# Performance work log

Hardware: AMD Instinct MI355X
Metric: run time of the kernel (lower is better)

The kernel has to match this reference:

```python
import jax, jax.numpy as jnp
import numpy as np

T, B, H = 1024, 256, 20


def setup_inputs() -> dict:
    key = jax.random.key(0)
    ks = jax.random.split(key, 6)

    def lin_w(k, fan_in, fan_out):
        bound = 1.0 / np.sqrt(fan_in)
        return jax.random.uniform(k, (fan_in, fan_out), jnp.float32, -bound, bound)

    # t is time-reversed (torch.flip): strictly decreasing, so dt = t[0]-t[1] > 0
    t = jnp.linspace(1.0, 0.0, T, dtype=jnp.float32).reshape(T, 1)
    y = jax.random.uniform(ks[0], (B, 1, 3), jnp.float32)  # initial SIR state per batch
    return {
        "t": t,
        "y": y,
        "w1": lin_w(ks[1], 1, H), "b1": jnp.zeros((H,), jnp.float32),
        "w2": lin_w(ks[2], H, H), "b2": jnp.zeros((H,), jnp.float32),
        "w3": lin_w(ks[3], H, H), "b3": jnp.zeros((H,), jnp.float32),
        "w4": lin_w(ks[4], H, 1), "b4": jnp.zeros((1,), jnp.float32),
        "beta": jnp.asarray(0.2, jnp.float32),
        "gamma": jnp.asarray(0.2, jnp.float32),
    }


def reference(t, y, w1, b1, w2, b2, w3, b3, w4, b4, beta, gamma):
    Tn = t.shape[0]
    dt = t[0, 0] - t[1, 0]  # positive scalar (t is reversed)

    # memory kernel me(t): Linear-Tanh x3 -> Linear-Sigmoid, shape [T]
    h = jnp.tanh(t @ w1 + b1)
    h = jnp.tanh(h @ w2 + b2)
    h = jnp.tanh(h @ w3 + b3)
    me = jax.nn.sigmoid(h @ w4 + b4)[:, 0]  # [T]
    # pad so me[-j:] can be read as a fixed-length dynamic slice (zeros past end)
    me_pad = jnp.concatenate([me, jnp.zeros((Tn,), me.dtype)])  # [2T]

    y0 = jnp.transpose(y, (1, 0, 2))[0]  # [B,3]  (y.transpose(1,0) then first/only row)
    Bn = y0.shape[0]
    # history buffer of I-compartment values; entries >= current length stay zero
    I_hist0 = jnp.zeros((Tn, Bn), y0.dtype).at[0].set(y0[:, 1])

    def step(carry, idx):
        y_cur, I_hist = carry  # y_cur [B,3], I_hist [T,B]
        j = idx + 1  # current solution length
        # kernel slice w[k] = me[T - j + k]; for k >= j both w (padding) and I_hist are 0
        w = jax.lax.dynamic_slice(me_pad, (Tn - j,), (Tn,))  # [T]
        integ = dt * jnp.einsum('t,tb->b', w, I_hist)  # memory integral, [B]
        S, I = y_cur[:, 0], y_cur[:, 1]
        bSI = beta * S * I
        gI = gamma * I
        d = jnp.stack([-bSI + integ, bSI - gI, gI - integ], axis=1)  # [B,3]
        y_next = y_cur + d * dt  # forward Euler
        I_hist = I_hist.at[j].set(y_next[:, 1])
        return (y_next, I_hist), (d, y_next)

    (_, _), (ds, ys) = jax.lax.scan(step, (y0, I_hist0), jnp.arange(Tn - 1))
    solution = jnp.concatenate([y0[None], ys], axis=0)  # [T,B,3]
    # original leaves diff[T-1] as zeros (loop fills rows 0..T-2)
    diff = jnp.concatenate([ds, jnp.zeros((1, Bn, 3), ds.dtype)], axis=0)  # [T,B,3]
    return solution, diff
```

## Files before the change

kernel.cpp:

```cpp
#include <hip/hip_runtime.h>

#define T_N 1024
#define B_N 256
#define H_N 20
#define NW  8
#define NDW (NW - 1)
#define SIH 1096

typedef _Float16 h8_t __attribute__((ext_vector_type(8)));

#if __has_builtin(__builtin_amdgcn_fdot2)
#define DOT8(acc, mv, iv)                                                           \
    acc = __builtin_amdgcn_fdot2(__builtin_shufflevector(mv, mv, 0, 1),             \
                                 __builtin_shufflevector(iv, iv, 0, 1), acc, false);\
    acc = __builtin_amdgcn_fdot2(__builtin_shufflevector(mv, mv, 2, 3),             \
                                 __builtin_shufflevector(iv, iv, 2, 3), acc, false);\
    acc = __builtin_amdgcn_fdot2(__builtin_shufflevector(mv, mv, 4, 5),             \
                                 __builtin_shufflevector(iv, iv, 4, 5), acc, false);\
    acc = __builtin_amdgcn_fdot2(__builtin_shufflevector(mv, mv, 6, 7),             \
                                 __builtin_shufflevector(iv, iv, 6, 7), acc, false);
#else
#define DOT8(acc, mv, iv)                                                           \
    _Pragma("unroll")                                                               \
    for (int _k = 0; _k < 8; ++_k) acc = fmaf((float)mv[_k], (float)iv[_k], acc);
#endif

__device__ __forceinline__ float rdlane_i(float v, int lane) {
    return __uint_as_float((unsigned)__builtin_amdgcn_readlane((int)__float_as_uint(v), lane));
}
__device__ __forceinline__ float fast_tanh(float x) {
    const float e = __expf(2.0f * x);
    return fmaf(-2.0f, __builtin_amdgcn_rcpf(e + 1.0f), 1.0f);
}
__device__ __forceinline__ float fast_sigmoid(float x) {
    return __builtin_amdgcn_rcpf(1.0f + __expf(-x));
}

#define REP64(F) \
    F(0) F(1) F(2) F(3) F(4) F(5) F(6) F(7) F(8) F(9) F(10) F(11) F(12) F(13) \
    F(14) F(15) F(16) F(17) F(18) F(19) F(20) F(21) F(22) F(23) F(24) F(25)   \
    F(26) F(27) F(28) F(29) F(30) F(31) F(32) F(33) F(34) F(35) F(36) F(37)   \
    F(38) F(39) F(40) F(41) F(42) F(43) F(44) F(45) F(46) F(47) F(48) F(49)   \
    F(50) F(51) F(52) F(53) F(54) F(55) F(56) F(57) F(58) F(59) F(60) F(61)   \
    F(62) F(63)

__global__ __launch_bounds__(512, 1) void me_kernel(
    const float* __restrict__ t,
    const float* __restrict__ w1, const float* __restrict__ b1,
    const float* __restrict__ w2, const float* __restrict__ b2,
    const float* __restrict__ w3, const float* __restrict__ b3,
    const float* __restrict__ w4, const float* __restrict__ b4,
    float* __restrict__ me_f,
    _Float16* __restrict__ me_h)
{
    const int gid = blockIdx.x * 512 + threadIdx.x;
    const float x = t[gid];

    float h1[H_N], h2[H_N];
#pragma unroll
    for (int k = 0; k < H_N; ++k) h1[k] = fast_tanh(fmaf(x, w1[k], b1[k]));

#pragma unroll 4
    for (int k = 0; k < H_N; ++k) {
        float a = b2[k];
#pragma unroll
        for (int j = 0; j < H_N; ++j) a = fmaf(h1[j], w2[j * H_N + k], a);
        h2[k] = fast_tanh(a);
    }

    float a4 = b4[0];
#pragma unroll 4
    for (int k = 0; k < H_N; ++k) {
        float a = b3[k];
#pragma unroll
        for (int j = 0; j < H_N; ++j) a = fmaf(h2[j], w3[j * H_N + k], a);
        a4 = fmaf(fast_tanh(a), w4[k], a4);
    }

    const float meval = fast_sigmoid(a4);
    me_f[gid] = meval;
    me_h[gid] = (_Float16)meval;
}

__global__ __launch_bounds__(512, 1) void scan_kernel(
    const float* __restrict__ me_f,
    const _Float16* __restrict__ me_h,
    const float* __restrict__ t,
    const float* __restrict__ y,
    const float* __restrict__ beta_p,
    const float* __restrict__ gamma_p,
    float* __restrict__ out)
{
    __shared__ __align__(16) float    sMeF[T_N];
    __shared__ __align__(16) _Float16 sMeH[T_N];
    __shared__ __align__(16) _Float16 sIhR[8 * SIH];
    __shared__ __align__(16) float    PA[2][64][4];
    __shared__ __align__(16) float    PB[2][64][4];

    const int b   = blockIdx.x;
    const int tid = threadIdx.x;
    const int wid = tid >> 6;
    const int L   = tid & 63;

    const int f    = (-L) & 7;
    const int R8   = L + f;
    const int row  = L & 7;
    const int iofs = row * SIH + (f ? 0 : 8);

    if (tid < 64) sIhR[(tid >> 3) * SIH + (tid & 7)] = (_Float16)0.0f;
    if (tid < 128) PB[tid >> 6][tid & 63][3] = 0.0f;

#pragma unroll
    for (int v = 0; v < 2; ++v) {
        const int mi = tid + v * 512;
        sMeF[mi] = me_f[mi];
        sMeH[mi] = me_h[mi];
    }

    const float dt    = t[0] - t[1];
    const float beta  = beta_p[0];
    const float gma   = gamma_p[0];
    const float invdt = 1.0f / dt;
    const float dt2   = dt * dt;

    const float S0 = y[b * 3 + 0];
    const float I0 = y[b * 3 + 1];
    const float R0 = y[b * 3 + 2];
    const float TOT = S0 + I0 + R0;

    if (tid < 8) sIhR[tid * SIH + 8 - tid] = (_Float16)I0;

    float* __restrict__ diff = out + (size_t)T_N * B_N * 3;
    if (tid < 3) diff[((size_t)(T_N - 1) * B_N + b) * 3 + tid] = 0.0f;

    __syncthreads();

    float mf[7];
#pragma unroll
    for (int d = 1; d <= 7; ++d) mf[d - 1] = sMeF[T_N - 64 - L - d];

    const float dtb   = dt * beta;
    const float ndtb  = -dtb;
    const float c1    = fmaf(-dt, gma, 1.0f);
    const float meT1s = dt2 * sMeF[T_N - 1];

    float S = S0, I = I0, oS = S0, oI = I0;
    float acc_cur = 0.0f, acc_nxt = 0.0f, pre = 0.0f;
    float carryS = S0, carryI = I0;

#define TBLDECL(k) float rm_##k, rn_##k;
    REP64(TBLDECL)
#undef TBLDECL
    if (wid == 0) {
#define TBLINIT(k)                                                          \
        rm_##k = (((k) < L) ? sMeF[T_N - L + (k)] : 0.0f) * dt2;            \
        rn_##k = dt2 * sMeF[T_N - 64 - L + (k)];
        REP64(TBLINIT)
#undef TBLINIT
#define TBLPIN(k) asm volatile("" : "+v"(rm_##k), "+v"(rn_##k));
        REP64(TBLPIN)
#undef TBLPIN
        __builtin_amdgcn_s_setprio(3);
    }

#define STEPB(M_, FIRST_)                                               \
    {                                                                   \
        const float sum = (FIRST_) ? pre : fmaf(meT1s, I, pre);         \
        float pnx = pre;                                                \
        if ((M_) < 63) pnx = rdlane_i(acc_cur, (M_) + 1);               \
        const float a  = fmaf(dtb, S, c1);                              \
        const float bb = fmaf(ndtb, I, 1.0f);                           \
        S = fmaf(bb, S, sum);                                           \
        I = I * a;                                                      \
        const bool cap = (L == (M_));                                   \
        oS = cap ? S : oS;                                              \
        oI = cap ? I : oI;                                              \
        acc_cur = fmaf(rm_##M_, I, acc_cur);                            \
        acc_nxt = fmaf(rn_##M_, I, acc_nxt);                            \
        pre = pnx;                                                      \
    }
#define STEP_GE1(M_) if ((M_) >= 1) STEPB(M_, false)
#define STEP_GE2(M_) if ((M_) >= 2) STEPB(M_, false)

    for (int c = 0; c < 16; ++c) {
        if (wid == 0) {
            if (c == 0) {
                acc_cur = rm_0 * I;
                acc_nxt = rn_0 * I;
                pre = rdlane_i(acc_cur, 1);
                STEPB(1, true)
                REP64(STEP_GE2)
            } else {
                const float4 pa = *(const float4*)&PA[c & 1][L][0];
                const float4 pb = *(const float4*)&PB[c & 1][L][0];
                const float ps = ((pa.x + pa.y) + (pa.z + pa.w)) +
                                 ((pb.x + pb.y) + (pb.z + pb.w));
                acc_cur = fmaf(dt2, ps, acc_nxt);
                acc_nxt = 0.0f;
                pre = rdlane_i(acc_cur, 0);
                STEPB(0, true)
                REP64(STEP_GE1)
            }

            const int j = 64 * c + L;
            const _Float16 hI = (_Float16)oI;
#pragma unroll
            for (int r = 0; r < 8; ++r) sIhR[r * SIH + 8 + (j - r)] = hI;

            const float oR = TOT - oS - oI;
            const size_t so = ((size_t)j * B_N + b) * 3;
            out[so + 0] = oS;
            out[so + 1] = oI;
            out[so + 2] = oR;

            float sm1 = __shfl_up(oS, 1);
            float im1 = __shfl_up(oI, 1);
            if (L == 0) { sm1 = carryS; im1 = carryI; }
            if (j > 0) {
                const float d0 = (oS - sm1) * invdt;
                const float d1 = (oI - im1) * invdt;
                const float d2 = -d0 - d1;
                const size_t dofs = ((size_t)(j - 1) * B_N + b) * 3;
                diff[dofs + 0] = d0;
                diff[dofs + 1] = d1;
                diff[dofs + 2] = d2;
            }
            carryS = rdlane_i(oS, 63);
            carryI = rdlane_i(oI, 63);
        } else if (c < 15) {
            const int w    = wid - 1;
            const int G    = 8 * c;
            const int idx0 = (T_N - 64 * (c + 1)) - R8;
            float p0 = 0.0f, p1 = 0.0f;
            int s = w;
            for (; s + NDW < G; s += 2 * NDW) {
                const h8_t mv0 = *(const h8_t*)&sMeH[idx0 + 8 * s];
                const h8_t iv0 = *(const h8_t*)&sIhR[iofs + 8 * s];
                const h8_t mv1 = *(const h8_t*)&sMeH[idx0 + 8 * (s + NDW)];
                const h8_t iv1 = *(const h8_t*)&sIhR[iofs + 8 * (s + NDW)];
                DOT8(p0, mv0, iv0)
                DOT8(p1, mv1, iv1)
            }
            if (s < G) {
                const h8_t mv0 = *(const h8_t*)&sMeH[idx0 + 8 * s];
                const h8_t iv0 = *(const h8_t*)&sIhR[iofs + 8 * s];
                DOT8(p0, mv0, iv0)
            }
            float p = p0 + p1;
            if (w == 0) {
#pragma unroll
                for (int d = 1; d <= 7; ++d) {
                    const float ih = (float)sIhR[8 + 64 * c - d];
                    if (d <= f) p = fmaf(mf[d - 1], ih, p);
                }
            }
            if (w < 4) PA[(c + 1) & 1][L][w] = p;
            else       PB[(c + 1) & 1][L][w - 4] = p;
        }
        __syncthreads();
    }
#undef STEPB
#undef STEP_GE1
#undef STEP_GE2
}

extern "C" void kernel_launch(void* const* d_in, const int* in_sizes, int n_in,
                              void* d_out, int out_size, void* d_ws, size_t ws_size,
                              hipStream_t stream) {
    const float* t     = (const float*)d_in[0];
    const float* y     = (const float*)d_in[1];
    const float* w1    = (const float*)d_in[2];
    const float* b1    = (const float*)d_in[3];
    const float* w2    = (const float*)d_in[4];
    const float* b2    = (const float*)d_in[5];
    const float* w3    = (const float*)d_in[6];
    const float* b3    = (const float*)d_in[7];
    const float* w4    = (const float*)d_in[8];
    const float* b4    = (const float*)d_in[9];
    const float* beta  = (const float*)d_in[10];
    const float* gamma = (const float*)d_in[11];

    float*    me_f = (float*)d_ws;
    _Float16* me_h = (_Float16*)((char*)d_ws + 4096);

    me_kernel<<<2, 512, 0, stream>>>(t, w1, b1, w2, b2, w3, b3, w4, b4, me_f, me_h);
    scan_kernel<<<B_N, 512, 0, stream>>>(me_f, me_h, t, y, beta, gamma, (float*)d_out);
}
```

Before: 114.2 us.

## Batch lane reads in groups of eight and patch the recent memory terms explicitly

Result: slower. 119.8 us (+4.9%).

```diff
diff --git a/kernel.cpp b/kernel.cpp
--- a/kernel.cpp
+++ b/kernel.cpp
@@ -143,10 +143,20 @@
     const float ndtb  = -dtb;
     const float c1    = fmaf(-dt, gma, 1.0f);
     const float meT1s = dt2 * sMeF[T_N - 1];
+    const float meT2s = dt2 * sMeF[T_N - 2];
+    const float meT3s = dt2 * sMeF[T_N - 3];
+    const float meT4s = dt2 * sMeF[T_N - 4];
+    const float meT5s = dt2 * sMeF[T_N - 5];
+    const float meT6s = dt2 * sMeF[T_N - 6];
+    const float meT7s = dt2 * sMeF[T_N - 7];
 
     float S = S0, I = I0, oS = S0, oI = I0;
-    float acc_cur = 0.0f, acc_nxt = 0.0f, pre = 0.0f;
+    float acc_cur = 0.0f, acc_nxt = 0.0f;
     float carryS = S0, carryI = I0;
+    float rd_0 = 0.0f, rd_1 = 0.0f, rd_2 = 0.0f, rd_3 = 0.0f;
+    float rd_4 = 0.0f, rd_5 = 0.0f, rd_6 = 0.0f, rd_7 = 0.0f;
+    float gi0 = 0.0f, gi1 = 0.0f, gi2 = 0.0f, gi3 = 0.0f;
+    float gi4 = 0.0f, gi5 = 0.0f, gi6 = 0.0f;
 
 #define TBLDECL(k) float rm_##k, rn_##k;
     REP64(TBLDECL)
@@ -163,11 +173,39 @@
         __builtin_amdgcn_s_setprio(3);
     }
 
-#define STEPB(M_, FIRST_)                                               \
+#define PATCH0(s_)
+#define PATCH1(s_) s_ = fmaf(meT1s, gi0, s_);
+#define PATCH2(s_) s_ = fmaf(meT1s, gi1, fmaf(meT2s, gi0, s_));
+#define PATCH3(s_) s_ = fmaf(meT1s, gi2, fmaf(meT2s, gi1, fmaf(meT3s, gi0, s_)));
+#define PATCH4(s_) s_ = fmaf(meT1s, gi3, fmaf(meT2s, gi2, fmaf(meT3s, gi1, \
+                        fmaf(meT4s, gi0, s_))));
+#define PATCH5(s_) s_ = fmaf(meT1s, gi4, fmaf(meT2s, gi3, fmaf(meT3s, gi2, \
+                        fmaf(meT4s, gi1, fmaf(meT5s, gi0, s_)))));
+#define PATCH6(s_) s_ = fmaf(meT1s, gi5, fmaf(meT2s, gi4, fmaf(meT3s, gi3, \
+                        fmaf(meT4s, gi2, fmaf(meT5s, gi1, fmaf(meT6s, gi0, s_))))));
+#define PATCH7(s_) s_ = fmaf(meT1s, gi6, fmaf(meT2s, gi5, fmaf(meT3s, gi4, \
+                        fmaf(meT4s, gi3, fmaf(meT5s, gi2, fmaf(meT6s, gi1, \
+                        fmaf(meT7s, gi0, s_)))))));
+
+#define GSTEP(M_, P_)                                                   \
     {                                                                   \
-        const float sum = (FIRST_) ? pre : fmaf(meT1s, I, pre);         \
-        float pnx = pre;                                                \
-        if ((M_) < 63) pnx = rdlane_i(acc_cur, (M_) + 1);               \
+        float sum = rd_##P_;                                            \
+        PATCH##P_(sum)                                                  \
+        const float a  = fmaf(dtb, S, c1);                              \
+        const float bb = fmaf(ndtb, I, 1.0f);                           \
+        S = fmaf(bb, S, sum);                                           \
+        I = I * a;                                                      \
+        gi##P_ = I;                                                     \
+        const bool cap = (L == (M_));                                   \
+        oS = cap ? S : oS;                                              \
+        oI = cap ? I : oI;                                              \
+        acc_cur = fmaf(rm_##M_, I, acc_cur);                            \
+        acc_nxt = fmaf(rn_##M_, I, acc_nxt);                            \
+    }
+#define GSTEP7(M_)                                                      \
+    {                                                                   \
+        float sum = rd_7;                                               \
+        PATCH7(sum)                                                     \
         const float a  = fmaf(dtb, S, c1);                              \
         const float bb = fmaf(ndtb, I, 1.0f);                           \
         S = fmaf(bb, S, sum);                                           \
@@ -177,19 +215,47 @@
         oI = cap ? I : oI;                                              \
         acc_cur = fmaf(rm_##M_, I, acc_cur);                            \
         acc_nxt = fmaf(rn_##M_, I, acc_nxt);                            \
-        pre = pnx;                                                      \
-    }
-#define STEP_GE1(M_) if ((M_) >= 1) STEPB(M_, false)
-#define STEP_GE2(M_) if ((M_) >= 2) STEPB(M_, false)
+    }
+
+#define GREAD(B_)                                                       \
+    rd_0 = rdlane_i(acc_cur, (B_) + 0);                                 \
+    rd_1 = rdlane_i(acc_cur, (B_) + 1);                                 \
+    rd_2 = rdlane_i(acc_cur, (B_) + 2);                                 \
+    rd_3 = rdlane_i(acc_cur, (B_) + 3);                                 \
+    rd_4 = rdlane_i(acc_cur, (B_) + 4);                                 \
+    rd_5 = rdlane_i(acc_cur, (B_) + 5);                                 \
+    rd_6 = rdlane_i(acc_cur, (B_) + 6);                                 \
+    rd_7 = rdlane_i(acc_cur, (B_) + 7);
+
+#define GROUP(B_, M0,M1,M2,M3,M4,M5,M6,M7)                              \
+    GREAD(B_)                                                           \
+    GSTEP(M0,0) GSTEP(M1,1) GSTEP(M2,2) GSTEP(M3,3)                     \
+    GSTEP(M4,4) GSTEP(M5,5) GSTEP(M6,6) GSTEP7(M7)
+
+#define GROUPS_8_63                                                     \
+    GROUP(8,  8,9,10,11,12,13,14,15)                                    \
+    GROUP(16, 16,17,18,19,20,21,22,23)                                  \
+    GROUP(24, 24,25,26,27,28,29,30,31)                                  \
+    GROUP(32, 32,33,34,35,36,37,38,39)                                  \
+    GROUP(40, 40,41,42,43,44,45,46,47)                                  \
+    GROUP(48, 48,49,50,51,52,53,54,55)                                  \
+    GROUP(56, 56,57,58,59,60,61,62,63)
 
     for (int c = 0; c < 16; ++c) {
         if (wid == 0) {
             if (c == 0) {
                 acc_cur = rm_0 * I;
                 acc_nxt = rn_0 * I;
-                pre = rdlane_i(acc_cur, 1);
-                STEPB(1, true)
-                REP64(STEP_GE2)
+                rd_0 = rdlane_i(acc_cur, 1);
+                rd_1 = rdlane_i(acc_cur, 2);
+                rd_2 = rdlane_i(acc_cur, 3);
+                rd_3 = rdlane_i(acc_cur, 4);
+                rd_4 = rdlane_i(acc_cur, 5);
+                rd_5 = rdlane_i(acc_cur, 6);
+                rd_6 = rdlane_i(acc_cur, 7);
+                GSTEP(1,0) GSTEP(2,1) GSTEP(3,2) GSTEP(4,3)
+                GSTEP(5,4) GSTEP(6,5) GSTEP(7,6)
+                GROUPS_8_63
             } else {
                 const float4 pa = *(const float4*)&PA[c & 1][L][0];
                 const float4 pb = *(const float4*)&PB[c & 1][L][0];
@@ -197,9 +263,8 @@
                                  ((pb.x + pb.y) + (pb.z + pb.w));
                 acc_cur = fmaf(dt2, ps, acc_nxt);
                 acc_nxt = 0.0f;
-                pre = rdlane_i(acc_cur, 0);
-                STEPB(0, true)
-                REP64(STEP_GE1)
+                GROUP(0, 0,1,2,3,4,5,6,7)
+                GROUPS_8_63
             }
 
             const int j = 64 * c + L;
@@ -259,9 +324,11 @@
         }
         __syncthreads();
     }
-#undef STEPB
-#undef STEP_GE1
-#undef STEP_GE2
+#undef GSTEP
+#undef GSTEP7
+#undef GREAD
+#undef GROUP
+#undef GROUPS_8_63
 }
 
 extern "C" void kernel_launch(void* const* d_in, const int* in_sizes, int n_in,
```
